# Optimization experiments

Measured on AMD Instinct MI355X. Metric: run time of the kernel, lower is better.

The kernel has to match this reference:

```python
import jax, jax.numpy as jnp
import numpy as np

N_EDGES = 4096
HIDDEN = 256
EDGE_DIM = 128
NUM_HEADS = 4
NUM_GRAPHS = 64


def setup_inputs() -> dict:
    key0 = jax.random.key(0)
    ks = jax.random.split(key0, 10)
    s = 0.02
    inp = {
        "query": jax.random.normal(ks[0], (N_EDGES, HIDDEN), jnp.float32),
        "key": jax.random.normal(ks[1], (N_EDGES, EDGE_DIM), jnp.float32),
        "value": jax.random.normal(ks[2], (N_EDGES, EDGE_DIM), jnp.float32),
        "edge_graph_index": jnp.sort(
            jax.random.randint(ks[3], (N_EDGES,), 0, NUM_GRAPHS)
        ),
        # edge_proj: Linear(edge_context_dim -> hidden_dim)
        "w_edge": jax.random.normal(ks[4], (HIDDEN, EDGE_DIM), jnp.float32) * s,
        "b_edge": jnp.zeros((HIDDEN,), jnp.float32),
        # nn.MultiheadAttention packed in-projection [3H, H] and bias [3H]
        "w_in": jax.random.normal(ks[5], (3 * HIDDEN, HIDDEN), jnp.float32) * s,
        "b_in": jnp.zeros((3 * HIDDEN,), jnp.float32),
        # out_proj: Linear(hidden -> hidden)
        "w_out": jax.random.normal(ks[6], (HIDDEN, HIDDEN), jnp.float32) * s,
        "b_out": jnp.zeros((HIDDEN,), jnp.float32),
    }
    return inp


def reference(query, key, value, edge_graph_index,
              w_edge, b_edge, w_in, b_in, w_out, b_out):
    # Segment-wise cross attention == block-diagonal masked attention over all edges.
    N, H = query.shape
    nh = NUM_HEADS
    dh = H // nh

    # edge feature projection (applied to both key and value, as in the module)
    K = key @ w_edge.T + b_edge      # [N, H]
    V = value @ w_edge.T + b_edge    # [N, H]

    wq, wk, wv = jnp.split(w_in, 3, axis=0)
    bq, bk, bv = jnp.split(b_in, 3)
    Qh = (query @ wq.T + bq).reshape(N, nh, dh)
    Kh = (K @ wk.T + bk).reshape(N, nh, dh)
    Vh = (V @ wv.T + bv).reshape(N, nh, dh)

    scale = 1.0 / jnp.sqrt(jnp.asarray(dh, query.dtype))
    scores = jnp.einsum("nhd,mhd->hnm", Qh, Kh) * scale  # [nh, N, N]

    # attention only within the same graph segment
    same_graph = edge_graph_index[:, None] == edge_graph_index[None, :]  # [N, N]
    neg = jnp.finfo(scores.dtype).min
    scores = jnp.where(same_graph[None, :, :], scores, neg)

    attn = jax.nn.softmax(scores, axis=-1)                 # [nh, N, N]
    out = jnp.einsum("hnm,mhd->nhd", attn, Vh).reshape(N, H)
    out = out @ w_out.T + b_out
    return query + out
```

## Files before the change

### kernel.cpp

```cpp
#include <hip/hip_runtime.h>

#define N_EDGES 4096
#define HIDDEN  256
#define EDGE_DIM 128
#define NUM_HEADS 4
#define NUM_GRAPHS 64
#define DH 64

typedef __attribute__((ext_vector_type(8))) short short8;
typedef __attribute__((ext_vector_type(4))) float f32x4;

__device__ __forceinline__ unsigned short f2bf(float f) {
  unsigned u = __builtin_bit_cast(unsigned, f);
  u += 0x7FFF + ((u >> 16) & 1);
  return (unsigned short)(u >> 16);
}
__device__ __forceinline__ float bf2f(unsigned short u) {
  return __builtin_bit_cast(float, (unsigned)u << 16);
}
__device__ __forceinline__ short8 cvt8(float4 x, float4 y) {
  short8 v;
  v[0] = (short)f2bf(x.x); v[1] = (short)f2bf(x.y);
  v[2] = (short)f2bf(x.z); v[3] = (short)f2bf(x.w);
  v[4] = (short)f2bf(y.x); v[5] = (short)f2bf(y.y);
  v[6] = (short)f2bf(y.z); v[7] = (short)f2bf(y.w);
  return v;
}

__device__ __forceinline__ int lbound(const int* __restrict__ a, int n, int v) {
  int lo = 0, hi = n;
  while (lo < hi) { int mid = (lo + hi) >> 1; if (a[mid] < v) lo = mid + 1; else hi = mid; }
  return lo;
}

template<bool ABF>
__device__ __forceinline__ void gemm_core(const void* Ap, const float* W,
                                          const float* bias, unsigned short* C,
                                          const int K) {
  const int t = threadIdx.x;
  const int m0 = blockIdx.x * 64, n0 = blockIdx.y * 64;
  __shared__ unsigned short As[64 * 40];
  __shared__ unsigned short Ws[64 * 40];
  const int r = t >> 2, kg = t & 3;
  const int lane = t & 63, w = t >> 6;
  const int quad = lane >> 4, l16 = lane & 15;
  const int wm = (w >> 1) * 32, wn = (w & 1) * 32;
  f32x4 acc[2][2] = {};
  const float* pw = W + (size_t)(n0 + r) * K + kg * 8;
  float4 w0 = *(const float4*)(pw), w1 = *(const float4*)(pw + 4);
  const unsigned short* pa16 = (const unsigned short*)Ap + (size_t)(m0 + r) * K + kg * 8;
  const float* pa32 = (const float*)Ap + (size_t)(m0 + r) * K + kg * 8;
  short8 a16; float4 a0, a1;
  if (ABF) a16 = *(const short8*)pa16;
  else { a0 = *(const float4*)pa32; a1 = *(const float4*)(pa32 + 4); }
  for (int kc = 0; kc < K; kc += 32) {
    short8 na16; float4 na0, na1, nw0, nw1;
    if (kc + 32 < K) {
      if (ABF) na16 = *(const short8*)(pa16 + kc + 32);
      else { na0 = *(const float4*)(pa32 + kc + 32); na1 = *(const float4*)(pa32 + kc + 36); }
      nw0 = *(const float4*)(pw + kc + 32); nw1 = *(const float4*)(pw + kc + 36);
    }
    __syncthreads();
    short8 av = ABF ? a16 : cvt8(a0, a1);
    *(short8*)&As[r * 40 + kg * 8] = av;
    *(short8*)&Ws[r * 40 + kg * 8] = cvt8(w0, w1);
    __syncthreads();
    short8 af0 = *(const short8*)&As[(wm + l16) * 40 + quad * 8];
    short8 af1 = *(const short8*)&As[(wm + 16 + l16) * 40 + quad * 8];
    short8 bf0 = *(const short8*)&Ws[(wn + l16) * 40 + quad * 8];
    short8 bf1 = *(const short8*)&Ws[(wn + 16 + l16) * 40 + quad * 8];
    acc[0][0] = __builtin_amdgcn_mfma_f32_16x16x32_bf16(af0, bf0, acc[0][0], 0, 0, 0);
    acc[0][1] = __builtin_amdgcn_mfma_f32_16x16x32_bf16(af0, bf1, acc[0][1], 0, 0, 0);
    acc[1][0] = __builtin_amdgcn_mfma_f32_16x16x32_bf16(af1, bf0, acc[1][0], 0, 0, 0);
    acc[1][1] = __builtin_amdgcn_mfma_f32_16x16x32_bf16(af1, bf1, acc[1][1], 0, 0, 0);
    a16 = na16; a0 = na0; a1 = na1; w0 = nw0; w1 = nw1;
  }
#pragma unroll
  for (int j = 0; j < 2; ++j) {
    const int col = n0 + wn + j * 16 + l16;
    const float bj = bias[col];
#pragma unroll
    for (int i = 0; i < 2; ++i) {
#pragma unroll
      for (int reg = 0; reg < 4; ++reg) {
        const int row = m0 + wm + i * 16 + quad * 4 + reg;
        C[(size_t)row * HIDDEN + col] = f2bf(acc[i][j][reg] + bj);
      }
    }
  }
}

__global__ __launch_bounds__(256) void proj1(const float* __restrict__ query,
                                             const float* __restrict__ key,
                                             const float* __restrict__ value,
                                             const float* __restrict__ w_in,
                                             const float* __restrict__ b_in,
                                             const float* __restrict__ w_edge,
                                             const float* __restrict__ b_edge,
                                             const int* __restrict__ gidx,
                                             unsigned short* Qh, unsigned short* Ek,
                                             unsigned short* Ev, int* segStart) {
  if (blockIdx.z == 0 && blockIdx.x == 0 && blockIdx.y == 0 && threadIdx.x <= NUM_GRAPHS)
    segStart[threadIdx.x] = lbound(gidx, N_EDGES, threadIdx.x);
  if (blockIdx.z == 0)      gemm_core<false>(query, w_in,   b_in,   Qh, 256);
  else if (blockIdx.z == 1) gemm_core<false>(key,   w_edge, b_edge, Ek, 128);
  else                      gemm_core<false>(value, w_edge, b_edge, Ev, 128);
}

__global__ __launch_bounds__(256) void proj2(const unsigned short* __restrict__ Ek,
                                             const unsigned short* __restrict__ Ev,
                                             const float* __restrict__ w_in,
                                             const float* __restrict__ b_in,
                                             unsigned short* Kh, unsigned short* Vh) {
  if (blockIdx.z == 0) gemm_core<true>(Ek, w_in + 256 * HIDDEN, b_in + 256, Kh, 256);
  else                 gemm_core<true>(Ev, w_in + 512 * HIDDEN, b_in + 512, Vh, 256);
}

__global__ __launch_bounds__(256) void attn_out(const unsigned short* __restrict__ Qh,
                                                const unsigned short* __restrict__ Kh,
                                                const unsigned short* __restrict__ Vh,
                                                const int* __restrict__ segStart,
                                                const float* __restrict__ w_out,
                                                const float* __restrict__ b_out,
                                                const float* __restrict__ query,
                                                float* __restrict__ out) {
  const int graph = blockIdx.x, zg = blockIdx.y;
  const int segLo = segStart[graph];
  const int segHi = segStart[graph + 1];
  const int segLen = segHi - segLo;
  const int t = threadIdx.x, lane = t & 63, w = t >> 6;
  const int quad = lane >> 4, l16 = lane & 15;
  __shared__ float Qs[16][260];
  __shared__ float Ks[64][68], Vs[64][68];
  __shared__ float Ps[4][64][4];
  __shared__ float ao[16][260];
  const float scale = 0.125f;
  const int r0 = w * 4;

  for (int chunk = zg; chunk * 16 < segLen; chunk += 8) {
    const int row0 = segLo + chunk * 16;
    const int rows = min(16, segHi - row0);
    __syncthreads();
#pragma unroll
    for (int it = 0; it < 2; ++it) {
      int s = t + it * 256; int r = s >> 5; int c8 = (s & 31) * 8;
      if (r < rows) {
        short8 q8 = *(const short8*)(Qh + (size_t)(row0 + r) * HIDDEN + c8);
        float4 f0, f1;
        f0.x = bf2f(q8[0]); f0.y = bf2f(q8[1]); f0.z = bf2f(q8[2]); f0.w = bf2f(q8[3]);
        f1.x = bf2f(q8[4]); f1.y = bf2f(q8[5]); f1.z = bf2f(q8[6]); f1.w = bf2f(q8[7]);
        *(float4*)&Qs[r][c8] = f0; *(float4*)&Qs[r][c8 + 4] = f1;
      }
    }

    for (int h = 0; h < NUM_HEADS; ++h) {
      float accv[4] = {0.f, 0.f, 0.f, 0.f}, lsum[4] = {0.f, 0.f, 0.f, 0.f};
      for (int c0 = segLo; c0 < segHi; c0 += 64) {
        const int tc = min(64, segHi - c0);
        __syncthreads();
#pragma unroll
        for (int it = 0; it < 2; ++it) {
          int s = t + it * 256; int j = s >> 3; int c8 = (s & 7) * 8;
          if (j < tc) {
            short8 k8 = *(const short8*)(Kh + (size_t)(c0 + j) * HIDDEN + h * DH + c8);
            short8 v8 = *(const short8*)(Vh + (size_t)(c0 + j) * HIDDEN + h * DH + c8);
#pragma unroll
            for (int e = 0; e < 8; ++e) Ks[j][c8 + e] = bf2f(k8[e]);
#pragma unroll
            for (int e = 0; e < 8; ++e) Vs[j][c8 + e] = bf2f(v8[e]);
          }
        }
        __syncthreads();
        float4 kreg[16];
#pragma unroll
        for (int d4 = 0; d4 < 16; ++d4) kreg[d4] = *(const float4*)&Ks[lane][d4 * 4];
        float p[4];
#pragma unroll
        for (int r = 0; r < 4; ++r) {
          float s = 0.f;
#pragma unroll
          for (int d4 = 0; d4 < 16; ++d4) {
            float4 q = *(const float4*)&Qs[r0 + r][h * DH + d4 * 4];
            s += q.x * kreg[d4].x + q.y * kreg[d4].y + q.z * kreg[d4].z + q.w * kreg[d4].w;
          }
          p[r] = (lane < tc && r0 + r < rows) ? __expf(s * scale) : 0.f;
          lsum[r] += p[r];
        }
        float4 p4; p4.x = p[0]; p4.y = p[1]; p4.z = p[2]; p4.w = p[3];
        *(float4*)&Ps[w][lane][0] = p4;
        __asm__ volatile("s_waitcnt lgkmcnt(0)" ::: "memory");
        for (int j = 0; j < tc; ++j) {
          const float v = Vs[j][lane];
          float4 pj = *(const float4*)&Ps[w][j][0];
          accv[0] += pj.x * v; accv[1] += pj.y * v;
          accv[2] += pj.z * v; accv[3] += pj.w * v;
        }
      }
#pragma unroll
      for (int off = 32; off; off >>= 1)
#pragma unroll
        for (int r = 0; r < 4; ++r) lsum[r] += __shfl_xor(lsum[r], off);
#pragma unroll
      for (int r = 0; r < 4; ++r)
        if (r0 + r < rows) ao[r0 + r][h * DH + lane] = accv[r] / lsum[r];
    }
    __syncthreads();

    const int wn = w * 64;
    f32x4 oc[4] = {};
    for (int kc = 0; kc < HIDDEN; kc += 32) {
      float4 a0 = *(const float4*)&ao[l16][kc + quad * 8];
      float4 a1 = *(const float4*)&ao[l16][kc + quad * 8 + 4];
      short8 af = cvt8(a0, a1);
#pragma unroll
      for (int nt = 0; nt < 4; ++nt) {
        const float* wr = w_out + (size_t)(wn + nt * 16 + l16) * HIDDEN + kc + quad * 8;
        short8 bf = cvt8(*(const float4*)wr, *(const float4*)(wr + 4));
        oc[nt] = __builtin_amdgcn_mfma_f32_16x16x32_bf16(af, bf, oc[nt], 0, 0, 0);
      }
    }
#pragma unroll
    for (int nt = 0; nt < 4; ++nt) {
      const int col = wn + nt * 16 + l16;
      const float bj = b_out[col];
#pragma unroll
      for (int reg = 0; reg < 4; ++reg) {
        const int m = quad * 4 + reg;
        if (m < rows) {
          const size_t idx = (size_t)(row0 + m) * HIDDEN + col;
          out[idx] = oc[nt][reg] + bj + query[idx];
        }
      }
    }
  }
}

extern "C" void kernel_launch(void* const* d_in, const int* in_sizes, int n_in,
                              void* d_out, int out_size, void* d_ws, size_t ws_size,
                              hipStream_t stream) {
  const float* query  = (const float*)d_in[0];
  const float* key    = (const float*)d_in[1];
  const float* value  = (const float*)d_in[2];
  const int*   gidx   = (const int*)d_in[3];
  const float* w_edge = (const float*)d_in[4];
  const float* b_edge = (const float*)d_in[5];
  const float* w_in   = (const float*)d_in[6];
  const float* b_in   = (const float*)d_in[7];
  const float* w_out  = (const float*)d_in[8];
  const float* b_out  = (const float*)d_in[9];
  float* out = (float*)d_out;

  int* segStart = (int*)d_ws;
  unsigned short* Qh = (unsigned short*)((char*)d_ws + 512);
  unsigned short* Ek = Qh + (size_t)N_EDGES * HIDDEN;
  unsigned short* Ev = Ek + (size_t)N_EDGES * HIDDEN;
  unsigned short* Kh = Ev + (size_t)N_EDGES * HIDDEN;
  unsigned short* Vh = Kh + (size_t)N_EDGES * HIDDEN;

  proj1<<<dim3(64, 4, 3), 256, 0, stream>>>(query, key, value, w_in, b_in,
                                            w_edge, b_edge, gidx, Qh, Ek, Ev, segStart);
  proj2<<<dim3(64, 4, 2), 256, 0, stream>>>(Ek, Ev, w_in, b_in, Kh, Vh);
  attn_out<<<dim3(NUM_GRAPHS, 8), 256, 0, stream>>>(Qh, Kh, Vh, segStart,
                                                    w_out, b_out, query, out);
}
```

Measured before the change: 144.1 us.

## Split attention per head across blocks and move out-projection to separate GEMM

The fused attention+out-projection kernel is split in two. The attention kernel now runs one block per (graph, head, chunk-group), which raises the grid from 512 to 2048 blocks and shrinks shared memory, and it writes a bf16 attention output to workspace. A separate tiled MFMA GEMM kernel then does the out-projection with bias and residual add. This removes the serial loop over heads and the per-chunk reloading of w_out, at the cost of an extra launch and a round trip of the attention output through global memory.

```diff
diff --git a/kernel.cpp b/kernel.cpp
--- a/kernel.cpp
+++ b/kernel.cpp
@@ -26,6 +26,11 @@
   v[6] = (short)f2bf(y.z); v[7] = (short)f2bf(y.w);
   return v;
 }
+__device__ __forceinline__ float4 us4f(ushort4 v) {
+  float4 f;
+  f.x = bf2f(v.x); f.y = bf2f(v.y); f.z = bf2f(v.z); f.w = bf2f(v.w);
+  return f;
+}
 
 __device__ __forceinline__ int lbound(const int* __restrict__ a, int n, int v) {
   int lo = 0, hi = n;
@@ -33,10 +38,10 @@
   return lo;
 }
 
-template<bool ABF>
+template<bool ABF, bool OUTF32>
 __device__ __forceinline__ void gemm_core(const void* Ap, const float* W,
-                                          const float* bias, unsigned short* C,
-                                          const int K) {
+                                          const float* bias, const float* res,
+                                          void* Cp, const int K) {
   const int t = threadIdx.x;
   const int m0 = blockIdx.x * 64, n0 = blockIdx.y * 64;
   __shared__ unsigned short As[64 * 40];
@@ -84,7 +89,10 @@
 #pragma unroll
       for (int reg = 0; reg < 4; ++reg) {
         const int row = m0 + wm + i * 16 + quad * 4 + reg;
-        C[(size_t)row * HIDDEN + col] = f2bf(acc[i][j][reg] + bj);
+        const size_t idx = (size_t)row * HIDDEN + col;
+        float v = acc[i][j][reg] + bj;
+        if (OUTF32) ((float*)Cp)[idx] = v + res[idx];
+        else        ((unsigned short*)Cp)[idx] = f2bf(v);
       }
     }
   }
@@ -102,9 +110,9 @@
                                              unsigned short* Ev, int* segStart) {
   if (blockIdx.z == 0 && blockIdx.x == 0 && blockIdx.y == 0 && threadIdx.x <= NUM_GRAPHS)
     segStart[threadIdx.x] = lbound(gidx, N_EDGES, threadIdx.x);
-  if (blockIdx.z == 0)      gemm_core<false>(query, w_in,   b_in,   Qh, 256);
-  else if (blockIdx.z == 1) gemm_core<false>(key,   w_edge, b_edge, Ek, 128);
-  else                      gemm_core<false>(value, w_edge, b_edge, Ev, 128);
+  if (blockIdx.z == 0)      gemm_core<false, false>(query, w_in,   b_in,   nullptr, Qh, 256);
+  else if (blockIdx.z == 1) gemm_core<false, false>(key,   w_edge, b_edge, nullptr, Ek, 128);
+  else                      gemm_core<false, false>(value, w_edge, b_edge, nullptr, Ev, 128);
 }
 
 __global__ __launch_bounds__(256) void proj2(const unsigned short* __restrict__ Ek,
@@ -112,28 +120,22 @@
                                              const float* __restrict__ w_in,
                                              const float* __restrict__ b_in,
                                              unsigned short* Kh, unsigned short* Vh) {
-  if (blockIdx.z == 0) gemm_core<true>(Ek, w_in + 256 * HIDDEN, b_in + 256, Kh, 256);
-  else                 gemm_core<true>(Ev, w_in + 512 * HIDDEN, b_in + 512, Vh, 256);
-}
-
-__global__ __launch_bounds__(256) void attn_out(const unsigned short* __restrict__ Qh,
-                                                const unsigned short* __restrict__ Kh,
-                                                const unsigned short* __restrict__ Vh,
-                                                const int* __restrict__ segStart,
-                                                const float* __restrict__ w_out,
-                                                const float* __restrict__ b_out,
-                                                const float* __restrict__ query,
-                                                float* __restrict__ out) {
-  const int graph = blockIdx.x, zg = blockIdx.y;
+  if (blockIdx.z == 0) gemm_core<true, false>(Ek, w_in + 256 * HIDDEN, b_in + 256, nullptr, Kh, 256);
+  else                 gemm_core<true, false>(Ev, w_in + 512 * HIDDEN, b_in + 512, nullptr, Vh, 256);
+}
+
+__global__ __launch_bounds__(256) void attn_segment(const unsigned short* __restrict__ Qh,
+                                                    const unsigned short* __restrict__ Kh,
+                                                    const unsigned short* __restrict__ Vh,
+                                                    const int* __restrict__ segStart,
+                                                    unsigned short* __restrict__ ao) {
+  const int graph = blockIdx.x, h = blockIdx.y, zg = blockIdx.z;
   const int segLo = segStart[graph];
   const int segHi = segStart[graph + 1];
   const int segLen = segHi - segLo;
   const int t = threadIdx.x, lane = t & 63, w = t >> 6;
-  const int quad = lane >> 4, l16 = lane & 15;
-  __shared__ float Qs[16][260];
-  __shared__ float Ks[64][68], Vs[64][68];
+  __shared__ float Qs[16][68], Ks[64][68], Vs[64][68];
   __shared__ float Ps[4][64][4];
-  __shared__ float ao[16][260];
   const float scale = 0.125f;
   const int r0 = w * 4;
 
@@ -141,98 +143,69 @@
     const int row0 = segLo + chunk * 16;
     const int rows = min(16, segHi - row0);
     __syncthreads();
-#pragma unroll
-    for (int it = 0; it < 2; ++it) {
-      int s = t + it * 256; int r = s >> 5; int c8 = (s & 31) * 8;
-      if (r < rows) {
-        short8 q8 = *(const short8*)(Qh + (size_t)(row0 + r) * HIDDEN + c8);
-        float4 f0, f1;
-        f0.x = bf2f(q8[0]); f0.y = bf2f(q8[1]); f0.z = bf2f(q8[2]); f0.w = bf2f(q8[3]);
-        f1.x = bf2f(q8[4]); f1.y = bf2f(q8[5]); f1.z = bf2f(q8[6]); f1.w = bf2f(q8[7]);
-        *(float4*)&Qs[r][c8] = f0; *(float4*)&Qs[r][c8 + 4] = f1;
+    { int r = t >> 4, d4 = (t & 15) * 4;
+      if (r < rows)
+        *(float4*)&Qs[r][d4] =
+            us4f(*(const ushort4*)(Qh + (size_t)(row0 + r) * HIDDEN + h * DH + d4)); }
+
+    float accv[4] = {0.f, 0.f, 0.f, 0.f}, lsum[4] = {0.f, 0.f, 0.f, 0.f};
+
+    for (int c0 = segLo; c0 < segHi; c0 += 64) {
+      const int tc = min(64, segHi - c0);
+      __syncthreads();
+#pragma unroll
+      for (int it = 0; it < 4; ++it) {
+        int s = t + it * 256; int j = s >> 4; int d4 = (s & 15) * 4;
+        if (j < tc) {
+          *(float4*)&Ks[j][d4] =
+              us4f(*(const ushort4*)(Kh + (size_t)(c0 + j) * HIDDEN + h * DH + d4));
+          *(float4*)&Vs[j][d4] =
+              us4f(*(const ushort4*)(Vh + (size_t)(c0 + j) * HIDDEN + h * DH + d4));
+        }
+      }
+      __syncthreads();
+      float4 kreg[16];
+#pragma unroll
+      for (int d4 = 0; d4 < 16; ++d4) kreg[d4] = *(const float4*)&Ks[lane][d4 * 4];
+      float p[4];
+#pragma unroll
+      for (int r = 0; r < 4; ++r) {
+        float s = 0.f;
+#pragma unroll
+        for (int d4 = 0; d4 < 16; ++d4) {
+          float4 q = *(const float4*)&Qs[r0 + r][d4 * 4];
+          s += q.x * kreg[d4].x + q.y * kreg[d4].y + q.z * kreg[d4].z + q.w * kreg[d4].w;
+        }
+        p[r] = (lane < tc && r0 + r < rows) ? __expf(s * scale) : 0.f;
+        lsum[r] += p[r];
+      }
+      float4 p4; p4.x = p[0]; p4.y = p[1]; p4.z = p[2]; p4.w = p[3];
+      *(float4*)&Ps[w][lane][0] = p4;
+      __asm__ volatile("s_waitcnt lgkmcnt(0)" ::: "memory");
+      for (int j = 0; j < tc; ++j) {
+        const float v = Vs[j][lane];
+        float4 pj = *(const float4*)&Ps[w][j][0];
+        accv[0] += pj.x * v; accv[1] += pj.y * v;
+        accv[2] += pj.z * v; accv[3] += pj.w * v;
       }
     }
-
-    for (int h = 0; h < NUM_HEADS; ++h) {
-      float accv[4] = {0.f, 0.f, 0.f, 0.f}, lsum[4] = {0.f, 0.f, 0.f, 0.f};
-      for (int c0 = segLo; c0 < segHi; c0 += 64) {
-        const int tc = min(64, segHi - c0);
-        __syncthreads();
-#pragma unroll
-        for (int it = 0; it < 2; ++it) {
-          int s = t + it * 256; int j = s >> 3; int c8 = (s & 7) * 8;
-          if (j < tc) {
-            short8 k8 = *(const short8*)(Kh + (size_t)(c0 + j) * HIDDEN + h * DH + c8);
-            short8 v8 = *(const short8*)(Vh + (size_t)(c0 + j) * HIDDEN + h * DH + c8);
-#pragma unroll
-            for (int e = 0; e < 8; ++e) Ks[j][c8 + e] = bf2f(k8[e]);
-#pragma unroll
-            for (int e = 0; e < 8; ++e) Vs[j][c8 + e] = bf2f(v8[e]);
-          }
-        }
-        __syncthreads();
-        float4 kreg[16];
-#pragma unroll
-        for (int d4 = 0; d4 < 16; ++d4) kreg[d4] = *(const float4*)&Ks[lane][d4 * 4];
-        float p[4];
-#pragma unroll
-        for (int r = 0; r < 4; ++r) {
-          float s = 0.f;
-#pragma unroll
-          for (int d4 = 0; d4 < 16; ++d4) {
-            float4 q = *(const float4*)&Qs[r0 + r][h * DH + d4 * 4];
-            s += q.x * kreg[d4].x + q.y * kreg[d4].y + q.z * kreg[d4].z + q.w * kreg[d4].w;
-          }
-          p[r] = (lane < tc && r0 + r < rows) ? __expf(s * scale) : 0.f;
-          lsum[r] += p[r];
-        }
-        float4 p4; p4.x = p[0]; p4.y = p[1]; p4.z = p[2]; p4.w = p[3];
-        *(float4*)&Ps[w][lane][0] = p4;
-        __asm__ volatile("s_waitcnt lgkmcnt(0)" ::: "memory");
-        for (int j = 0; j < tc; ++j) {
-          const float v = Vs[j][lane];
-          float4 pj = *(const float4*)&Ps[w][j][0];
-          accv[0] += pj.x * v; accv[1] += pj.y * v;
-          accv[2] += pj.z * v; accv[3] += pj.w * v;
-        }
-      }
-#pragma unroll
-      for (int off = 32; off; off >>= 1)
-#pragma unroll
-        for (int r = 0; r < 4; ++r) lsum[r] += __shfl_xor(lsum[r], off);
-#pragma unroll
-      for (int r = 0; r < 4; ++r)
-        if (r0 + r < rows) ao[r0 + r][h * DH + lane] = accv[r] / lsum[r];
-    }
-    __syncthreads();
-
-    const int wn = w * 64;
-    f32x4 oc[4] = {};
-    for (int kc = 0; kc < HIDDEN; kc += 32) {
-      float4 a0 = *(const float4*)&ao[l16][kc + quad * 8];
-      float4 a1 = *(const float4*)&ao[l16][kc + quad * 8 + 4];
-      short8 af = cvt8(a0, a1);
-#pragma unroll
-      for (int nt = 0; nt < 4; ++nt) {
-        const float* wr = w_out + (size_t)(wn + nt * 16 + l16) * HIDDEN + kc + quad * 8;
-        short8 bf = cvt8(*(const float4*)wr, *(const float4*)(wr + 4));
-        oc[nt] = __builtin_amdgcn_mfma_f32_16x16x32_bf16(af, bf, oc[nt], 0, 0, 0);
-      }
-    }
-#pragma unroll
-    for (int nt = 0; nt < 4; ++nt) {
-      const int col = wn + nt * 16 + l16;
-      const float bj = b_out[col];
-#pragma unroll
-      for (int reg = 0; reg < 4; ++reg) {
-        const int m = quad * 4 + reg;
-        if (m < rows) {
-          const size_t idx = (size_t)(row0 + m) * HIDDEN + col;
-          out[idx] = oc[nt][reg] + bj + query[idx];
-        }
-      }
-    }
+#pragma unroll
+    for (int off = 32; off; off >>= 1)
+#pragma unroll
+      for (int r = 0; r < 4; ++r) lsum[r] += __shfl_xor(lsum[r], off);
+#pragma unroll
+    for (int r = 0; r < 4; ++r)
+      if (r0 + r < rows)
+        ao[(size_t)(row0 + r0 + r) * HIDDEN + h * DH + lane] = f2bf(accv[r] / lsum[r]);
   }
+}
+
+__global__ __launch_bounds__(256) void outproj(const unsigned short* __restrict__ ao,
+                                               const float* __restrict__ w_out,
+                                               const float* __restrict__ b_out,
+                                               const float* __restrict__ query,
+                                               float* __restrict__ out) {
+  gemm_core<true, true>(ao, w_out, b_out, query, out, 256);
 }
 
 extern "C" void kernel_launch(void* const* d_in, const int* in_sizes, int n_in,
@@ -256,10 +229,11 @@
   unsigned short* Ev = Ek + (size_t)N_EDGES * HIDDEN;
   unsigned short* Kh = Ev + (size_t)N_EDGES * HIDDEN;
   unsigned short* Vh = Kh + (size_t)N_EDGES * HIDDEN;
+  unsigned short* ao = Vh + (size_t)N_EDGES * HIDDEN;
 
   proj1<<<dim3(64, 4, 3), 256, 0, stream>>>(query, key, value, w_in, b_in,
                                             w_edge, b_edge, gidx, Qh, Ek, Ev, segStart);
   proj2<<<dim3(64, 4, 2), 256, 0, stream>>>(Ek, Ev, w_in, b_in, Kh, Vh);
-  attn_out<<<dim3(NUM_GRAPHS, 8), 256, 0, stream>>>(Qh, Kh, Vh, segStart,
-                                                    w_out, b_out, query, out);
-}
+  attn_segment<<<dim3(NUM_GRAPHS, NUM_HEADS, 8), 256, 0, stream>>>(Qh, Kh, Vh, segStart, ao);
+  outproj<<<dim3(64, 4), 256, 0, stream>>>(ao, w_out, b_out, query, out);
+}
```

Result: faster. 117.9 us (-18.2%).
